# Performance work log

Hardware: AMD Instinct MI355X
Metric: run time of the kernel (lower is better)

Reference implementation:

```python
import jax, jax.numpy as jnp
import numpy as np

N = 50000   # num_nodes
E = 400000  # num_edges
IN, HID, OUT, H = 128, 64, 128, 4
GAT_HID = HID * H  # 256
EPS = 1e-5
NEG_SLOPE = 0.2


def setup_inputs() -> dict:
    key = jax.random.key(0)
    ks = jax.random.split(key, 24)

    def w(k, shape, fan_in):
        return (jax.random.normal(k, shape) * (1.0 / np.sqrt(fan_in))).astype(jnp.float32)

    x = jax.random.normal(ks[0], (N, IN), dtype=jnp.float32)
    edge_index = jax.random.randint(ks[1], (2, E), 0, N, dtype=jnp.int32)

    return {
        "x": x,
        "edge_index": edge_index,
        # GCN branch: layer1 IN->HID, layer2 HID->OUT
        "W_gcn1": w(ks[2], (IN, HID), IN), "b_gcn1": jnp.zeros((HID,), jnp.float32),
        "W_gcn2": w(ks[3], (HID, OUT), HID), "b_gcn2": jnp.zeros((OUT,), jnp.float32),
        # GAT branch: layer1 IN -> H heads x HID (concat), layer2 GAT_HID -> H heads x OUT (mean)
        "W_gat1": w(ks[4], (IN, H * HID), IN),
        "a_src1": w(ks[5], (H, HID), HID), "a_dst1": w(ks[6], (H, HID), HID),
        "b_gat1": jnp.zeros((H * HID,), jnp.float32),
        "W_gat2": w(ks[7], (GAT_HID, H * OUT), GAT_HID),
        "a_src2": w(ks[8], (H, OUT), OUT), "a_dst2": w(ks[9], (H, OUT), OUT),
        "b_gat2": jnp.zeros((OUT,), jnp.float32),
        # LayerNorms
        "g_gcn": jnp.ones((OUT,), jnp.float32), "bt_gcn": jnp.zeros((OUT,), jnp.float32),
        "g_gat": jnp.ones((OUT,), jnp.float32), "bt_gat": jnp.zeros((OUT,), jnp.float32),
        # projected_concat fusion
        "W_fuse": w(ks[10], (2 * OUT, OUT), 2 * OUT), "b_fuse": jnp.zeros((OUT,), jnp.float32),
    }


def _with_self_loops(src, dst, n):
    loop = jnp.arange(n, dtype=src.dtype)
    return jnp.concatenate([src, loop]), jnp.concatenate([dst, loop])


def _gcn_layer(x, W, b, src, dst, n):
    # PyG GCNConv: x' = D^{-1/2}(A+I)D^{-1/2} X W + b
    xw = x @ W
    s, d = _with_self_loops(src, dst, n)
    deg = jax.ops.segment_sum(jnp.ones_like(s, dtype=xw.dtype), d, num_segments=n)
    dis = jnp.where(deg > 0, jax.lax.rsqrt(jnp.maximum(deg, 1.0)), 0.0)
    norm = dis[s] * dis[d]                      # [E2]
    msg = norm[:, None] * xw[s]                 # [E2, C]
    return jax.ops.segment_sum(msg, d, num_segments=n) + b


def _segment_softmax(e, seg, n):
    m = jax.ops.segment_max(e, seg, num_segments=n)
    ee = jnp.exp(e - m[seg])
    den = jax.ops.segment_sum(ee, seg, num_segments=n)
    return ee / den[seg]


def _gat_layer(x, W, a_src, a_dst, b, src, dst, n, heads, out_ch, concat):
    xh = (x @ W).reshape(n, heads, out_ch)      # [N, H, C]
    alpha_s = jnp.einsum('nhc,hc->nh', xh, a_src)
    alpha_d = jnp.einsum('nhc,hc->nh', xh, a_dst)
    s, d = _with_self_loops(src, dst, n)
    e = jax.nn.leaky_relu(alpha_s[s] + alpha_d[d], NEG_SLOPE)   # [E2, H]
    alpha = _segment_softmax(e, d, n)                           # [E2, H]
    out = jax.ops.segment_sum(alpha[:, :, None] * xh[s], d, num_segments=n)  # [N,H,C]
    if concat:
        return out.reshape(n, heads * out_ch) + b
    return out.mean(axis=1) + b


def _layer_norm(x, g, b):
    mu = x.mean(axis=-1, keepdims=True)
    var = ((x - mu) ** 2).mean(axis=-1, keepdims=True)
    return (x - mu) * jax.lax.rsqrt(var + EPS) * g + b


def reference(x, edge_index,
              W_gcn1, b_gcn1, W_gcn2, b_gcn2,
              W_gat1, a_src1, a_dst1, b_gat1,
              W_gat2, a_src2, a_dst2, b_gat2,
              g_gcn, bt_gcn, g_gat, bt_gat,
              W_fuse, b_fuse):
    src, dst = edge_index[0], edge_index[1]
    n = x.shape[0]
    # GCN branch (relu between layers, dropout p=0.0 -> identity)
    h = jax.nn.relu(_gcn_layer(x, W_gcn1, b_gcn1, src, dst, n))
    x_gcn = _gcn_layer(h, W_gcn2, b_gcn2, src, dst, n)
    # GAT branch (elu between layers)
    g1 = _gat_layer(x, W_gat1, a_src1, a_dst1, b_gat1, src, dst, n, H, HID, True)
    g1 = jax.nn.elu(g1)
    x_gat = _gat_layer(g1, W_gat2, a_src2, a_dst2, b_gat2, src, dst, n, H, OUT, False)
    # Norm + projected_concat fusion
    x_gcn = _layer_norm(x_gcn, g_gcn, bt_gcn)
    x_gat = _layer_norm(x_gat, g_gat, bt_gat)
    x_cat = jnp.concatenate([x_gcn, x_gat], axis=-1)
    return x_cat @ W_fuse + b_fuse
```

## Files before the change

### kernel.cpp

```cpp
#include <hip/hip_runtime.h>
#include <cmath>

static constexpr float EPS = 1e-5f;
static constexpr float NEG = 0.2f;

typedef __attribute__((ext_vector_type(8))) short short8v;
typedef __attribute__((ext_vector_type(4))) short short4v;
typedef __attribute__((ext_vector_type(4))) float f32x4;
typedef __attribute__((ext_vector_type(2))) float f32x2;

__device__ inline unsigned short f2bf(float f) {
    union { float f; unsigned u; } v; v.f = f;
    unsigned r = v.u + 0x7FFF + ((v.u >> 16) & 1);
    return (unsigned short)(r >> 16);
}
__device__ inline float bf2f(unsigned short u) {
    union { unsigned u; float f; } v; v.u = (unsigned)u << 16; return v.f;
}

__global__ void setup_kernel(const int* __restrict__ ei, int* __restrict__ cnt, int E, int n,
                             const float* __restrict__ x, unsigned short* __restrict__ xb,
                             const float* W1, const float* W2, const float* W3,
                             const float* W4, const float* W5,
                             unsigned short* T1, unsigned short* T2, unsigned short* T3,
                             unsigned short* TF, unsigned short* T5,
                             const float* as1, const float* ad1,
                             const float* as2, const float* ad2,
                             float* wa1, float* wa2) {
    int gid = blockIdx.x * 256 + threadIdx.x;
    if (gid < E) {
        atomicAdd(&cnt[ei[E + gid]], 1);
        return;
    }
    gid -= E;
    int n32 = n * 32;
    if (gid < n32) {
        float4 v = *reinterpret_cast<const float4*>(&x[(size_t)gid * 4]);
        unsigned long long pk = (unsigned long long)f2bf(v.x)
                              | ((unsigned long long)f2bf(v.y) << 16)
                              | ((unsigned long long)f2bf(v.z) << 32)
                              | ((unsigned long long)f2bf(v.w) << 48);
        *reinterpret_cast<unsigned long long*>(&xb[(size_t)gid * 4]) = pk;
        return;
    }
    gid -= n32;
    if (gid < 212992) {
        int idx = gid;
        if (idx < 8192) {
            int c = idx / 128, k = idx % 128;
            T1[idx] = f2bf(W1[(size_t)k * 64 + c]);
        } else if (idx < 16384) {
            int j = idx - 8192, c = j / 64, k = j % 64;
            T2[j] = f2bf(W2[(size_t)k * 128 + c]);
        } else if (idx < 49152) {
            int j = idx - 16384, c = j / 128, k = j % 128;
            T3[j] = f2bf(W3[(size_t)k * 256 + c]);
        } else if (idx < 180224) {
            int j = idx - 49152;
            int c = j / 1024, kk = j % 1024, h = kk >> 8, k = kk & 255;
            TF[j] = f2bf(0.25f * W4[(size_t)k * 512 + h * 128 + c]);
        } else {
            int j = idx - 180224, c = j / 256, k = j % 256;
            T5[j] = f2bf(W5[(size_t)k * 128 + c]);
        }
        return;
    }
    gid -= 212992;
    if (gid < 1024) {
        int k = gid >> 3, t = gid & 7, h = t >> 1;
        const float* a = (t & 1) ? ad1 : as1;
        float s = 0.f;
        for (int c = 0; c < 64; c++) s += W3[(size_t)k * 256 + h * 64 + c] * a[h * 64 + c];
        wa1[gid] = s;
    } else if (gid < 3072) {
        int j = gid - 1024;
        int k = j >> 3, t = j & 7, h = t >> 1;
        const float* a = (t & 1) ? ad2 : as2;
        float s = 0.f;
        for (int c = 0; c < 128; c++) s += W4[(size_t)k * 512 + h * 128 + c] * a[h * 128 + c];
        wa2[j] = s;
    }
}

__global__ __launch_bounds__(256) void partial_kernel(const int* __restrict__ cnt,
                                                      int* __restrict__ partials, int n) {
    int tid = threadIdx.x, lane = tid & 63, wid = tid >> 6;
    int base = blockIdx.x * 1024 + tid * 4;
    int s = 0;
    if (base + 3 < n) {
        int4 v = *reinterpret_cast<const int4*>(&cnt[base]);
        s = v.x + v.y + v.z + v.w;
    } else {
        for (int j = 0; j < 4; j++) if (base + j < n) s += cnt[base + j];
    }
    #pragma unroll
    for (int o = 32; o; o >>= 1) s += __shfl_xor(s, o, 64);
    __shared__ int ws[4];
    if (lane == 0) ws[wid] = s;
    __syncthreads();
    if (tid == 0) partials[blockIdx.x] = ws[0] + ws[1] + ws[2] + ws[3];
}

__global__ void scanp_kernel(int* __restrict__ partials, int nb) {
    int lane = threadIdx.x;
    int v = (lane < nb) ? partials[lane] : 0;
    int s = v;
    #pragma unroll
    for (int o = 1; o < 64; o <<= 1) {
        int t = __shfl_up(s, o, 64);
        if (lane >= o) s += t;
    }
    if (lane < nb) partials[lane] = s - v;
}

__global__ __launch_bounds__(256) void scan2_kernel(const int* __restrict__ cnt,
                                                    const int* __restrict__ partials,
                                                    int* __restrict__ rowptr,
                                                    int* __restrict__ cursor,
                                                    float* __restrict__ dis, int n, int E) {
    int tid = threadIdx.x, lane = tid & 63, wid = tid >> 6;
    int base = blockIdx.x * 1024 + tid * 4;
    int v[4]; int s = 0;
    #pragma unroll
    for (int j = 0; j < 4; j++) { v[j] = (base + j < n) ? cnt[base + j] : 0; s += v[j]; }
    int ts = s;
    #pragma unroll
    for (int o = 1; o < 64; o <<= 1) {
        int t = __shfl_up(ts, o, 64);
        if (lane >= o) ts += t;
    }
    __shared__ int wsum[4];
    if (lane == 63) wsum[wid] = ts;
    __syncthreads();
    int woff = 0;
    for (int w = 0; w < wid; w++) woff += wsum[w];
    int excl = ts - s + woff + partials[blockIdx.x];
    #pragma unroll
    for (int j = 0; j < 4; j++) {
        int idx = base + j;
        if (idx < n) {
            rowptr[idx] = excl;
            cursor[idx] = excl;
            dis[idx] = rsqrtf((float)(v[j] + 1));
            excl += v[j];
        }
    }
    if (blockIdx.x == 0 && tid == 0) rowptr[n] = E;
}

__global__ void fill_kernel(const int* __restrict__ ei, int* __restrict__ cursor,
                            int* __restrict__ col, int E) {
    int e = blockIdx.x * 256 + threadIdx.x;
    if (e < E) {
        int d = ei[E + e];
        int pos = atomicAdd(&cursor[d], 1);
        col[pos] = ei[e];
    }
}

template<int BM, int K, int C, bool OBF, int ACT>
__global__ __launch_bounds__(256) void mfma_gemm(const unsigned short* __restrict__ A,
                                                 const unsigned short* __restrict__ WT,
                                                 const float* __restrict__ bias,
                                                 void* __restrict__ outp, int M) {
    constexpr int BN = 64, BK = 64;
    constexpr int MF = BM / 64;
    __shared__ unsigned short As[BM * BK];
    __shared__ unsigned short Ws[BN * BK];
    int tid = threadIdx.x;
    int wid = tid >> 6, lane = tid & 63;
    int m0 = blockIdx.x * BM;
    int n0 = blockIdx.y * BN;

    f32x4 acc[MF][4] = {};

    for (int k0 = 0; k0 < K; k0 += BK) {
        for (int i = tid; i < BM * (BK / 8); i += 256) {
            int row = i >> 3;
            int kk = (i & 7) * 8;
            int gr = m0 + row;
            short8v v = short8v{0, 0, 0, 0, 0, 0, 0, 0};
            if (gr < M) v = *reinterpret_cast<const short8v*>(&A[(size_t)gr * K + k0 + kk]);
            int byte = (kk * 2) ^ ((row & 7) << 4);
            *reinterpret_cast<short8v*>((char*)As + row * (BK * 2) + byte) = v;
        }
        for (int i = tid; i < BN * (BK / 8); i += 256) {
            int nrow = i >> 3;
            int kk = (i & 7) * 8;
            short8v v = *reinterpret_cast<const short8v*>(&WT[(size_t)(n0 + nrow) * K + k0 + kk]);
            int byte = (kk * 2) ^ ((nrow & 7) << 4);
            *reinterpret_cast<short8v*>((char*)Ws + nrow * (BK * 2) + byte) = v;
        }
        __syncthreads();
        #pragma unroll
        for (int kc = 0; kc < BK; kc += 32) {
            short8v afr[MF], bfr[4];
            int kk = kc + (lane >> 4) * 8;
            #pragma unroll
            for (int mf = 0; mf < MF; mf++) {
                int row = wid * (16 * MF) + mf * 16 + (lane & 15);
                int byte = (kk * 2) ^ ((row & 7) << 4);
                afr[mf] = *reinterpret_cast<const short8v*>((char*)As + row * (BK * 2) + byte);
            }
            #pragma unroll
            for (int nf = 0; nf < 4; nf++) {
                int nrow = nf * 16 + (lane & 15);
                int byte = (kk * 2) ^ ((nrow & 7) << 4);
                bfr[nf] = *reinterpret_cast<const short8v*>((char*)Ws + nrow * (BK * 2) + byte);
            }
            #pragma unroll
            for (int mf = 0; mf < MF; mf++)
                #pragma unroll
                for (int nf = 0; nf < 4; nf++)
                    acc[mf][nf] = __builtin_amdgcn_mfma_f32_16x16x32_bf16(
                        afr[mf], bfr[nf], acc[mf][nf], 0, 0, 0);
        }
        __syncthreads();
    }
    #pragma unroll
    for (int mf = 0; mf < MF; mf++) {
        #pragma unroll
        for (int nf = 0; nf < 4; nf++) {
            #pragma unroll
            for (int r = 0; r < 4; r++) {
                int row = m0 + wid * (16 * MF) + mf * 16 + (lane >> 4) * 4 + r;
                int colg = n0 + nf * 16 + (lane & 15);
                if (row < M) {
                    float v = acc[mf][nf][r];
                    if (bias) v += bias[colg];
                    if (ACT == 1) v = fmaxf(v, 0.f);
                    if constexpr (OBF)
                        ((unsigned short*)outp)[(size_t)row * C + colg] = f2bf(v);
                    else
                        ((float*)outp)[(size_t)row * C + colg] = v;
                }
            }
        }
    }
}

__global__ __launch_bounds__(256) void gemm_head_kernel(const unsigned short* __restrict__ A,
                                                        const unsigned short* __restrict__ WT3,
                                                        const float* __restrict__ bias,
                                                        unsigned short* __restrict__ g1b, int M) {
    constexpr int BM = 64, BK = 64, K = 128;
    int head = blockIdx.y;
    __shared__ unsigned short As[BM * BK];
    __shared__ unsigned short Ws[64 * BK];
    int tid = threadIdx.x;
    int wid = tid >> 6, lane = tid & 63;
    int m0 = blockIdx.x * BM;

    f32x4 acc[4] = {};

    for (int k0 = 0; k0 < K; k0 += BK) {
        for (int i = tid; i < BM * (BK / 8); i += 256) {
            int row = i >> 3;
            int kk = (i & 7) * 8;
            int gr = m0 + row;
            short8v v = short8v{0, 0, 0, 0, 0, 0, 0, 0};
            if (gr < M) v = *reinterpret_cast<const short8v*>(&A[(size_t)gr * 512 + head * 128 + k0 + kk]);
            int byte = (kk * 2) ^ ((row & 7) << 4);
            *reinterpret_cast<short8v*>((char*)As + row * (BK * 2) + byte) = v;
        }
        for (int i = tid; i < 64 * (BK / 8); i += 256) {
            int nrow = i >> 3;
            int kk = (i & 7) * 8;
            short8v v = *reinterpret_cast<const short8v*>(&WT3[(size_t)(head * 64 + nrow) * 128 + k0 + kk]);
            int byte = (kk * 2) ^ ((nrow & 7) << 4);
            *reinterpret_cast<short8v*>((char*)Ws + nrow * (BK * 2) + byte) = v;
        }
        __syncthreads();
        #pragma unroll
        for (int kc = 0; kc < BK; kc += 32) {
            short8v afr, bfr[4];
            int kk = kc + (lane >> 4) * 8;
            {
                int row = wid * 16 + (lane & 15);
                int byte = (kk * 2) ^ ((row & 7) << 4);
                afr = *reinterpret_cast<const short8v*>((char*)As + row * (BK * 2) + byte);
            }
            #pragma unroll
            for (int nf = 0; nf < 4; nf++) {
                int nrow = nf * 16 + (lane & 15);
                int byte = (kk * 2) ^ ((nrow & 7) << 4);
                bfr[nf] = *reinterpret_cast<const short8v*>((char*)Ws + nrow * (BK * 2) + byte);
            }
            #pragma unroll
            for (int nf = 0; nf < 4; nf++)
                acc[nf] = __builtin_amdgcn_mfma_f32_16x16x32_bf16(afr, bfr[nf], acc[nf], 0, 0, 0);
        }
        __syncthreads();
    }
    #pragma unroll
    for (int nf = 0; nf < 4; nf++) {
        #pragma unroll
        for (int r = 0; r < 4; r++) {
            int row = m0 + wid * 16 + (lane >> 4) * 4 + r;
            int cl = head * 64 + nf * 16 + (lane & 15);
            if (row < M) {
                float v = acc[nf][r] + bias[cl];
                v = v > 0.f ? v : __expf(v) - 1.f;
                g1b[(size_t)row * 256 + cl] = f2bf(v);
            }
        }
    }
}

template<int K>
__global__ __launch_bounds__(256) void gemm_ln_kernel(const unsigned short* __restrict__ A,
                                                      const unsigned short* __restrict__ WT,
                                                      const float* __restrict__ bias,
                                                      const float* __restrict__ gw,
                                                      const float* __restrict__ gb,
                                                      unsigned short* __restrict__ catb,
                                                      int coloff, int M) {
    constexpr int BM = 64, BN = 128, BK = 64;
    __shared__ unsigned short As[BM * BK];
    __shared__ unsigned short Ws[BN * BK];
    int tid = threadIdx.x;
    int wid = tid >> 6, lane = tid & 63;
    int m0 = blockIdx.x * BM;

    f32x4 acc[8] = {};

    for (int k0 = 0; k0 < K; k0 += BK) {
        for (int i = tid; i < BM * (BK / 8); i += 256) {
            int row = i >> 3;
            int kk = (i & 7) * 8;
            int gr = m0 + row;
            short8v v = short8v{0, 0, 0, 0, 0, 0, 0, 0};
            if (gr < M) v = *reinterpret_cast<const short8v*>(&A[(size_t)gr * K + k0 + kk]);
            int byte = (kk * 2) ^ ((row & 7) << 4);
            *reinterpret_cast<short8v*>((char*)As + row * (BK * 2) + byte) = v;
        }
        for (int i = tid; i < BN * (BK / 8); i += 256) {
            int nrow = i >> 3;
            int kk = (i & 7) * 8;
            short8v v = *reinterpret_cast<const short8v*>(&WT[(size_t)nrow * K + k0 + kk]);
            int byte = (kk * 2) ^ ((nrow & 7) << 4);
            *reinterpret_cast<short8v*>((char*)Ws + nrow * (BK * 2) + byte) = v;
        }
        __syncthreads();
        #pragma unroll
        for (int kc = 0; kc < BK; kc += 32) {
            short8v afr, bfr[8];
            int kk = kc + (lane >> 4) * 8;
            {
                int row = wid * 16 + (lane & 15);
                int byte = (kk * 2) ^ ((row & 7) << 4);
                afr = *reinterpret_cast<const short8v*>((char*)As + row * (BK * 2) + byte);
            }
            #pragma unroll
            for (int nf = 0; nf < 8; nf++) {
                int nrow = nf * 16 + (lane & 15);
                int byte = (kk * 2) ^ ((nrow & 7) << 4);
                bfr[nf] = *reinterpret_cast<const short8v*>((char*)Ws + nrow * (BK * 2) + byte);
            }
            #pragma unroll
            for (int nf = 0; nf < 8; nf++)
                acc[nf] = __builtin_amdgcn_mfma_f32_16x16x32_bf16(afr, bfr[nf], acc[nf], 0, 0, 0);
        }
        __syncthreads();
    }
    int cb = lane & 15;
    float gwv[8], gbv[8], bv[8];
    #pragma unroll
    for (int nf = 0; nf < 8; nf++) {
        int c = nf * 16 + cb;
        gwv[nf] = gw[c]; gbv[nf] = gb[c]; bv[nf] = bias[c];
    }
    #pragma unroll
    for (int r = 0; r < 4; r++) {
        int row = m0 + wid * 16 + (lane >> 4) * 4 + r;
        float v[8]; float sm = 0.f, sq = 0.f;
        #pragma unroll
        for (int nf = 0; nf < 8; nf++) {
            v[nf] = acc[nf][r] + bv[nf];
            sm += v[nf]; sq += v[nf] * v[nf];
        }
        #pragma unroll
        for (int o = 1; o < 16; o <<= 1) { sm += __shfl_xor(sm, o, 64); sq += __shfl_xor(sq, o, 64); }
        float mu = sm * (1.f / 128.f);
        float var = sq * (1.f / 128.f) - mu * mu;
        float rs = rsqrtf(var + EPS);
        if (row < M) {
            #pragma unroll
            for (int nf = 0; nf < 8; nf++)
                catb[(size_t)row * 256 + coloff + nf * 16 + cb] =
                    f2bf((v[nf] - mu) * rs * gwv[nf] + gbv[nf]);
        }
    }
}

template<int K>
__global__ __launch_bounds__(256) void alpha_x_kernel(const unsigned short* __restrict__ F,
                                                      const float* __restrict__ wa,
                                                      float* __restrict__ as_, float* __restrict__ ad_, int n) {
    constexpr int PL = K / 64;
    int wid = threadIdx.x >> 6, lane = threadIdx.x & 63;
    int node = blockIdx.x * 4 + wid;
    if (node >= n) return;
    float p[8] = {0, 0, 0, 0, 0, 0, 0, 0};
    const unsigned short* fr = F + (size_t)node * K + lane * PL;
    #pragma unroll
    for (int j = 0; j < PL; j++) {
        float v = bf2f(fr[j]);
        const float4* w4 = reinterpret_cast<const float4*>(wa + (size_t)(lane * PL + j) * 8);
        float4 wA = w4[0], wB = w4[1];
        p[0] += v * wA.x; p[1] += v * wA.y; p[2] += v * wA.z; p[3] += v * wA.w;
        p[4] += v * wB.x; p[5] += v * wB.y; p[6] += v * wB.z; p[7] += v * wB.w;
    }
    #pragma unroll
    for (int o = 1; o < 64; o <<= 1) {
        #pragma unroll
        for (int t = 0; t < 8; t++) p[t] += __shfl_xor(p[t], o, 64);
    }
    if (lane == 0) {
        #pragma unroll
        for (int t = 0; t < 8; t++) {
            if (t & 1) ad_[(size_t)node * 4 + (t >> 1)] = p[t];
            else       as_[(size_t)node * 4 + (t >> 1)] = p[t];
        }
    }
}

__global__ __launch_bounds__(256) void prop1_agg1_kernel(const unsigned short* __restrict__ xb,
                                                         const float* __restrict__ dis,
                                                         const float* __restrict__ as_,
                                                         const float* __restrict__ ad_,
                                                         const int* __restrict__ rowptr,
                                                         const int* __restrict__ col,
                                                         unsigned short* __restrict__ aggx,
                                                         unsigned short* __restrict__ agg,
                                                         int n) {
    constexpr int CAP = 96;
    __shared__ float ex[4][CAP][4];
    __shared__ float dsl[4][CAP];
    __shared__ int scol[4][CAP];
    int wid = threadIdx.x >> 6, lane = threadIdx.x & 63;
    int node = blockIdx.x * 4 + wid;
    if (node >= n) return;
    int b0 = rowptr[node];
    int cnt = rowptr[node + 1] - b0;
    float4 adv = *reinterpret_cast<const float4*>(&ad_[(size_t)node * 4]);
    float p0 = 0, p1 = 0, p2 = 0, p3 = 0;
    for (int i = lane; i <= cnt; i += 64) {
        int s = (i == cnt) ? node : col[b0 + i];
        float4 asv = *reinterpret_cast<const float4*>(&as_[(size_t)s * 4]);
        float e0 = asv.x + adv.x; e0 = e0 > 0.f ? e0 : NEG * e0; float x0 = __expf(e0);
        float e1 = asv.y + adv.y; e1 = e1 > 0.f ? e1 : NEG * e1; float x1 = __expf(e1);
        float e2 = asv.z + adv.z; e2 = e2 > 0.f ? e2 : NEG * e2; float x2 = __expf(e2);
        float e3 = asv.w + adv.w; e3 = e3 > 0.f ? e3 : NEG * e3; float x3 = __expf(e3);
        if (i < CAP) {
            ex[wid][i][0] = x0; ex[wid][i][1] = x1; ex[wid][i][2] = x2; ex[wid][i][3] = x3;
            scol[wid][i] = s;
            dsl[wid][i] = dis[s];
        }
        p0 += x0; p1 += x1; p2 += x2; p3 += x3;
    }
    #pragma unroll
    for (int o = 1; o < 64; o <<= 1) {
        p0 += __shfl_xor(p0, o, 64); p1 += __shfl_xor(p1, o, 64);
        p2 += __shfl_xor(p2, o, 64); p3 += __shfl_xor(p3, o, 64);
    }
    float inv0 = 1.f / p0, inv1 = 1.f / p1, inv2 = 1.f / p2, inv3 = 1.f / p3;
    for (int i = lane; i <= cnt && i < CAP; i += 64) {
        ex[wid][i][0] *= inv0; ex[wid][i][1] *= inv1;
        ex[wid][i][2] *= inv2; ex[wid][i][3] *= inv3;
    }
    __builtin_amdgcn_wave_barrier();
    f32x2 g2 = {0.f, 0.f};
    f32x2 ac2[4] = {};
    for (int i = 0; i <= cnt; i++) {
        int s; float w0, w1, w2, w3, dsv;
        if (i < CAP) {
            s = scol[wid][i];
            float4 e = *reinterpret_cast<const float4*>(&ex[wid][i][0]);
            w0 = e.x; w1 = e.y; w2 = e.z; w3 = e.w;
            dsv = dsl[wid][i];
        } else {
            s = (i == cnt) ? node : col[b0 + i];
            float4 asv = *reinterpret_cast<const float4*>(&as_[(size_t)s * 4]);
            float e0 = asv.x + adv.x; e0 = e0 > 0.f ? e0 : NEG * e0;
            float e1 = asv.y + adv.y; e1 = e1 > 0.f ? e1 : NEG * e1;
            float e2 = asv.z + adv.z; e2 = e2 > 0.f ? e2 : NEG * e2;
            float e3 = asv.w + adv.w; e3 = e3 > 0.f ? e3 : NEG * e3;
            w0 = __expf(e0) * inv0; w1 = __expf(e1) * inv1;
            w2 = __expf(e2) * inv2; w3 = __expf(e3) * inv3;
            dsv = dis[s];
        }
        unsigned gv = *reinterpret_cast<const unsigned*>(&xb[(size_t)s * 128 + lane * 2]);
        f32x2 f;
        f.x = bf2f((unsigned short)(gv & 0xFFFF));
        f.y = bf2f((unsigned short)(gv >> 16));
        g2 += dsv * f;
        ac2[0] += w0 * f;
        ac2[1] += w1 * f;
        ac2[2] += w2 * f;
        ac2[3] += w3 * f;
    }
    float dd = dis[node];
    unsigned pkg = (unsigned)f2bf(dd * g2.x) | ((unsigned)f2bf(dd * g2.y) << 16);
    *reinterpret_cast<unsigned*>(&aggx[(size_t)node * 128 + lane * 2]) = pkg;
    #pragma unroll
    for (int h = 0; h < 4; h++) {
        unsigned pk = (unsigned)f2bf(ac2[h].x) | ((unsigned)f2bf(ac2[h].y) << 16);
        *reinterpret_cast<unsigned*>(&agg[(size_t)node * 512 + h * 128 + lane * 2]) = pk;
    }
}

__global__ __launch_bounds__(256) void prop2_agg2_kernel(const unsigned short* __restrict__ g1b,
                                                         const unsigned short* __restrict__ hb,
                                                         const float* __restrict__ dis,
                                                         const float* __restrict__ as_,
                                                         const float* __restrict__ ad_,
                                                         const int* __restrict__ rowptr,
                                                         const int* __restrict__ col,
                                                         unsigned short* __restrict__ aggh,
                                                         unsigned short* __restrict__ agg,
                                                         int n) {
    constexpr int CAP = 96;
    __shared__ float ex[4][CAP][4];
    __shared__ float dsl[4][CAP];
    __shared__ int scol[4][CAP];
    int wid = threadIdx.x >> 6, lane = threadIdx.x & 63;
    int node = blockIdx.x * 4 + wid;
    if (node >= n) return;
    int b0 = rowptr[node];
    int cnt = rowptr[node + 1] - b0;
    float4 adv = *reinterpret_cast<const float4*>(&ad_[(size_t)node * 4]);
    float p0 = 0, p1 = 0, p2 = 0, p3 = 0;
    for (int i = lane; i <= cnt; i += 64) {
        int s = (i == cnt) ? node : col[b0 + i];
        float4 asv = *reinterpret_cast<const float4*>(&as_[(size_t)s * 4]);
        float e0 = asv.x + adv.x; e0 = e0 > 0.f ? e0 : NEG * e0; float x0 = __expf(e0);
        float e1 = asv.y + adv.y; e1 = e1 > 0.f ? e1 : NEG * e1; float x1 = __expf(e1);
        float e2 = asv.z + adv.z; e2 = e2 > 0.f ? e2 : NEG * e2; float x2 = __expf(e2);
        float e3 = asv.w + adv.w; e3 = e3 > 0.f ? e3 : NEG * e3; float x3 = __expf(e3);
        if (i < CAP) {
            ex[wid][i][0] = x0; ex[wid][i][1] = x1; ex[wid][i][2] = x2; ex[wid][i][3] = x3;
            scol[wid][i] = s;
            dsl[wid][i] = dis[s];
        }
        p0 += x0; p1 += x1; p2 += x2; p3 += x3;
    }
    #pragma unroll
    for (int o = 1; o < 64; o <<= 1) {
        p0 += __shfl_xor(p0, o, 64); p1 += __shfl_xor(p1, o, 64);
        p2 += __shfl_xor(p2, o, 64); p3 += __shfl_xor(p3, o, 64);
    }
    float inv0 = 1.f / p0, inv1 = 1.f / p1, inv2 = 1.f / p2, inv3 = 1.f / p3;
    for (int i = lane; i <= cnt && i < CAP; i += 64) {
        ex[wid][i][0] *= inv0; ex[wid][i][1] *= inv1;
        ex[wid][i][2] *= inv2; ex[wid][i][3] *= inv3;
    }
    __builtin_amdgcn_wave_barrier();
    float hacc = 0.f;
    f32x2 ac2[4][2] = {};
    for (int i = 0; i <= cnt; i++) {
        int s; float w0, w1, w2, w3, dsv;
        if (i < CAP) {
            s = scol[wid][i];
            float4 e = *reinterpret_cast<const float4*>(&ex[wid][i][0]);
            w0 = e.x; w1 = e.y; w2 = e.z; w3 = e.w;
            dsv = dsl[wid][i];
        } else {
            s = (i == cnt) ? node : col[b0 + i];
            float4 asv = *reinterpret_cast<const float4*>(&as_[(size_t)s * 4]);
            float e0 = asv.x + adv.x; e0 = e0 > 0.f ? e0 : NEG * e0;
            float e1 = asv.y + adv.y; e1 = e1 > 0.f ? e1 : NEG * e1;
            float e2 = asv.z + adv.z; e2 = e2 > 0.f ? e2 : NEG * e2;
            float e3 = asv.w + adv.w; e3 = e3 > 0.f ? e3 : NEG * e3;
            w0 = __expf(e0) * inv0; w1 = __expf(e1) * inv1;
            w2 = __expf(e2) * inv2; w3 = __expf(e3) * inv3;
            dsv = dis[s];
        }
        short4v v = *reinterpret_cast<const short4v*>(&g1b[(size_t)s * 256 + lane * 4]);
        float hv = bf2f(hb[(size_t)s * 64 + lane]);
        hacc += dsv * hv;
        f32x2 fa, fb;
        fa.x = bf2f((unsigned short)v[0]); fa.y = bf2f((unsigned short)v[1]);
        fb.x = bf2f((unsigned short)v[2]); fb.y = bf2f((unsigned short)v[3]);
        ac2[0][0] += w0 * fa; ac2[0][1] += w0 * fb;
        ac2[1][0] += w1 * fa; ac2[1][1] += w1 * fb;
        ac2[2][0] += w2 * fa; ac2[2][1] += w2 * fb;
        ac2[3][0] += w3 * fa; ac2[3][1] += w3 * fb;
    }
    float dd = dis[node];
    aggh[(size_t)node * 64 + lane] = f2bf(dd * hacc);
    #pragma unroll
    for (int h = 0; h < 4; h++) {
        short4v o4;
        o4[0] = (short)f2bf(ac2[h][0].x); o4[1] = (short)f2bf(ac2[h][0].y);
        o4[2] = (short)f2bf(ac2[h][1].x); o4[3] = (short)f2bf(ac2[h][1].y);
        *reinterpret_cast<short4v*>(&agg[(size_t)node * 1024 + h * 256 + lane * 4]) = o4;
    }
}

extern "C" void kernel_launch(void* const* d_in, const int* in_sizes, int n_in,
                              void* d_out, int out_size, void* d_ws, size_t ws_size,
                              hipStream_t stream) {
    const float* x      = (const float*)d_in[0];
    const int*   ei     = (const int*)d_in[1];
    const float* W_gcn1 = (const float*)d_in[2];
    const float* b_gcn1 = (const float*)d_in[3];
    const float* W_gcn2 = (const float*)d_in[4];
    const float* b_gcn2 = (const float*)d_in[5];
    const float* W_gat1 = (const float*)d_in[6];
    const float* a_src1 = (const float*)d_in[7];
    const float* a_dst1 = (const float*)d_in[8];
    const float* b_gat1 = (const float*)d_in[9];
    const float* W_gat2 = (const float*)d_in[10];
    const float* a_src2 = (const float*)d_in[11];
    const float* a_dst2 = (const float*)d_in[12];
    const float* b_gat2 = (const float*)d_in[13];
    const float* g_gcn  = (const float*)d_in[14];
    const float* bt_gcn = (const float*)d_in[15];
    const float* g_gat  = (const float*)d_in[16];
    const float* bt_gat = (const float*)d_in[17];
    const float* W_fuse = (const float*)d_in[18];
    const float* b_fuse = (const float*)d_in[19];
    float* out = (float*)d_out;

    const int n = in_sizes[0] / 128;
    const int E = in_sizes[1] / 2;

    char* ws = (char*)d_ws;
    size_t off = 0;
    auto alloc = [&](size_t bytes) -> char* {
        char* p = ws + off;
        off += (bytes + 255) & ~(size_t)255;
        return p;
    };
    int*   cnt      = (int*)alloc((size_t)n * 4);
    int*   rowptr   = (int*)alloc((size_t)(n + 1) * 4);
    int*   cursor   = (int*)alloc((size_t)n * 4);
    int*   col      = (int*)alloc((size_t)E * 4);
    int*   partials = (int*)alloc(64 * 4);
    float* dis      = (float*)alloc((size_t)n * 4);
    float* as_      = (float*)alloc((size_t)n * 16);
    float* ad_      = (float*)alloc((size_t)n * 16);
    float* wa1      = (float*)alloc(1024 * 4);
    float* wa2      = (float*)alloc(2048 * 4);
    unsigned short* xb   = (unsigned short*)alloc((size_t)n * 128 * 2);
    unsigned short* WT1  = (unsigned short*)alloc(8192 * 2);
    unsigned short* WT2  = (unsigned short*)alloc(8192 * 2);
    unsigned short* WT3  = (unsigned short*)alloc(32768 * 2);
    unsigned short* WTF  = (unsigned short*)alloc(131072 * 2);
    unsigned short* WT5  = (unsigned short*)alloc(32768 * 2);
    unsigned short* BIG   = (unsigned short*)alloc((size_t)n * 1024 * 2);
    unsigned short* agg2b = BIG;
    unsigned short* agg1b = BIG;
    unsigned short* aggx1 = BIG + (size_t)n * 512;
    unsigned short* hb    = (unsigned short*)alloc((size_t)n * 64 * 2);
    unsigned short* aggh  = (unsigned short*)alloc((size_t)n * 64 * 2);
    unsigned short* g1b   = (unsigned short*)alloc((size_t)n * 256 * 2);
    unsigned short* catb  = (unsigned short*)alloc((size_t)n * 256 * 2);

    const int nb = (n + 1023) / 1024;

    hipMemsetAsync(cnt, 0, (size_t)n * 4, stream);
    {
        long long total = (long long)E + (long long)n * 32 + 212992 + 3072;
        int blocks = (int)((total + 255) / 256);
        setup_kernel<<<blocks, 256, 0, stream>>>(ei, cnt, E, n, x, xb,
            W_gcn1, W_gcn2, W_gat1, W_gat2, W_fuse, WT1, WT2, WT3, WTF, WT5,
            a_src1, a_dst1, a_src2, a_dst2, wa1, wa2);
    }
    partial_kernel<<<nb, 256, 0, stream>>>(cnt, partials, n);
    scanp_kernel<<<1, 64, 0, stream>>>(partials, nb);
    scan2_kernel<<<nb, 256, 0, stream>>>(cnt, partials, rowptr, cursor, dis, n, E);
    fill_kernel<<<(E + 255) / 256, 256, 0, stream>>>(ei, cursor, col, E);

    int gm64 = (n + 63) / 64;
    int gn4 = (n + 3) / 4;

    alpha_x_kernel<128><<<gn4, 256, 0, stream>>>(xb, wa1, as_, ad_, n);
    prop1_agg1_kernel<<<gn4, 256, 0, stream>>>(xb, dis, as_, ad_, rowptr, col, aggx1, agg1b, n);
    mfma_gemm<64, 128, 64, true, 1><<<dim3(gm64, 1), 256, 0, stream>>>(aggx1, WT1, b_gcn1, hb, n);
    gemm_head_kernel<<<dim3(gm64, 4), 256, 0, stream>>>(agg1b, WT3, b_gat1, g1b, n);
    alpha_x_kernel<256><<<gn4, 256, 0, stream>>>(g1b, wa2, as_, ad_, n);
    prop2_agg2_kernel<<<gn4, 256, 0, stream>>>(g1b, hb, dis, as_, ad_, rowptr, col, aggh, agg2b, n);
    gemm_ln_kernel<64><<<gm64, 256, 0, stream>>>(aggh, WT2, b_gcn2, g_gcn, bt_gcn, catb, 0, n);
    gemm_ln_kernel<1024><<<gm64, 256, 0, stream>>>(agg2b, WTF, b_gat2, g_gat, bt_gat, catb, 128, n);

    mfma_gemm<64, 256, 128, false, 0><<<dim3(gm64, 2), 256, 0, stream>>>(catb, WT5, b_fuse, out, n);
}
```

Measured before the change: 351.2 us.

## Unroll gather loops by two and prescale GCN hidden by source degree norm

The two propagation kernels now process two neighbours per iteration, issuing both gathers before accumulating so more memory loads are in flight. In prop2 the per-edge dis[s] multiply is removed by folding the source normalisation into the first GEMM epilogue through a new rowscale argument. The shared-memory cache of dis values is dropped and the LDS cache capacity shrinks from 96 to 64 entries, which may raise occupancy. The cost is that nodes above 64 neighbours take the recompute path more often, and prop1 now reads dis[s] from global memory on every edge.

```diff
diff --git a/kernel.cpp b/kernel.cpp
--- a/kernel.cpp
+++ b/kernel.cpp
@@ -162,6 +162,7 @@
 __global__ __launch_bounds__(256) void mfma_gemm(const unsigned short* __restrict__ A,
                                                  const unsigned short* __restrict__ WT,
                                                  const float* __restrict__ bias,
+                                                 const float* __restrict__ rowscale,
                                                  void* __restrict__ outp, int M) {
     constexpr int BN = 64, BK = 64;
     constexpr int MF = BM / 64;
@@ -229,6 +230,7 @@
                     float v = acc[mf][nf][r];
                     if (bias) v += bias[colg];
                     if (ACT == 1) v = fmaxf(v, 0.f);
+                    if (rowscale) v *= rowscale[row];
                     if constexpr (OBF)
                         ((unsigned short*)outp)[(size_t)row * C + colg] = f2bf(v);
                     else
@@ -434,9 +436,8 @@
                                                          unsigned short* __restrict__ aggx,
                                                          unsigned short* __restrict__ agg,
                                                          int n) {
-    constexpr int CAP = 96;
+    constexpr int CAP = 64;
     __shared__ float ex[4][CAP][4];
-    __shared__ float dsl[4][CAP];
     __shared__ int scol[4][CAP];
     int wid = threadIdx.x >> 6, lane = threadIdx.x & 63;
     int node = blockIdx.x * 4 + wid;
@@ -455,7 +456,6 @@
         if (i < CAP) {
             ex[wid][i][0] = x0; ex[wid][i][1] = x1; ex[wid][i][2] = x2; ex[wid][i][3] = x3;
             scol[wid][i] = s;
-            dsl[wid][i] = dis[s];
         }
         p0 += x0; p1 += x1; p2 += x2; p3 += x3;
     }
@@ -470,15 +470,11 @@
         ex[wid][i][2] *= inv2; ex[wid][i][3] *= inv3;
     }
     __builtin_amdgcn_wave_barrier();
-    f32x2 g2 = {0.f, 0.f};
-    f32x2 ac2[4] = {};
-    for (int i = 0; i <= cnt; i++) {
-        int s; float w0, w1, w2, w3, dsv;
+
+    auto fetchw = [&](int i, int &s, float4 &w) {
         if (i < CAP) {
             s = scol[wid][i];
-            float4 e = *reinterpret_cast<const float4*>(&ex[wid][i][0]);
-            w0 = e.x; w1 = e.y; w2 = e.z; w3 = e.w;
-            dsv = dsl[wid][i];
+            w = *reinterpret_cast<const float4*>(&ex[wid][i][0]);
         } else {
             s = (i == cnt) ? node : col[b0 + i];
             float4 asv = *reinterpret_cast<const float4*>(&as_[(size_t)s * 4]);
@@ -486,19 +482,41 @@
             float e1 = asv.y + adv.y; e1 = e1 > 0.f ? e1 : NEG * e1;
             float e2 = asv.z + adv.z; e2 = e2 > 0.f ? e2 : NEG * e2;
             float e3 = asv.w + adv.w; e3 = e3 > 0.f ? e3 : NEG * e3;
-            w0 = __expf(e0) * inv0; w1 = __expf(e1) * inv1;
-            w2 = __expf(e2) * inv2; w3 = __expf(e3) * inv3;
-            dsv = dis[s];
-        }
-        unsigned gv = *reinterpret_cast<const unsigned*>(&xb[(size_t)s * 128 + lane * 2]);
-        f32x2 f;
-        f.x = bf2f((unsigned short)(gv & 0xFFFF));
-        f.y = bf2f((unsigned short)(gv >> 16));
-        g2 += dsv * f;
-        ac2[0] += w0 * f;
-        ac2[1] += w1 * f;
-        ac2[2] += w2 * f;
-        ac2[3] += w3 * f;
+            w = make_float4(__expf(e0) * inv0, __expf(e1) * inv1,
+                            __expf(e2) * inv2, __expf(e3) * inv3);
+        }
+    };
+
+    f32x2 g2 = {0.f, 0.f};
+    f32x2 ac2[4] = {};
+    int total = cnt + 1;
+    int i = 0;
+    for (; i + 1 < total; i += 2) {
+        int s0, s1; float4 wa, wb;
+        fetchw(i, s0, wa);
+        fetchw(i + 1, s1, wb);
+        float ds0 = dis[s0], ds1 = dis[s1];
+        unsigned gv0 = *reinterpret_cast<const unsigned*>(&xb[(size_t)s0 * 128 + lane * 2]);
+        unsigned gv1 = *reinterpret_cast<const unsigned*>(&xb[(size_t)s1 * 128 + lane * 2]);
+        f32x2 f0, f1;
+        f0.x = bf2f((unsigned short)(gv0 & 0xFFFF)); f0.y = bf2f((unsigned short)(gv0 >> 16));
+        f1.x = bf2f((unsigned short)(gv1 & 0xFFFF)); f1.y = bf2f((unsigned short)(gv1 >> 16));
+        g2 += ds0 * f0;      g2 += ds1 * f1;
+        ac2[0] += wa.x * f0; ac2[0] += wb.x * f1;
+        ac2[1] += wa.y * f0; ac2[1] += wb.y * f1;
+        ac2[2] += wa.z * f0; ac2[2] += wb.z * f1;
+        ac2[3] += wa.w * f0; ac2[3] += wb.w * f1;
+    }
+    if (i < total) {
+        int s0; float4 wa;
+        fetchw(i, s0, wa);
+        float ds0 = dis[s0];
+        unsigned gv0 = *reinterpret_cast<const unsigned*>(&xb[(size_t)s0 * 128 + lane * 2]);
+        f32x2 f0;
+        f0.x = bf2f((unsigned short)(gv0 & 0xFFFF)); f0.y = bf2f((unsigned short)(gv0 >> 16));
+        g2 += ds0 * f0;
+        ac2[0] += wa.x * f0; ac2[1] += wa.y * f0;
+        ac2[2] += wa.z * f0; ac2[3] += wa.w * f0;
     }
     float dd = dis[node];
     unsigned pkg = (unsigned)f2bf(dd * g2.x) | ((unsigned)f2bf(dd * g2.y) << 16);
@@ -511,7 +529,7 @@
 }
 
 __global__ __launch_bounds__(256) void prop2_agg2_kernel(const unsigned short* __restrict__ g1b,
-                                                         const unsigned short* __restrict__ hb,
+                                                         const unsigned short* __restrict__ hbs,
                                                          const float* __restrict__ dis,
                                                          const float* __restrict__ as_,
                                                          const float* __restrict__ ad_,
@@ -520,9 +538,8 @@
                                                          unsigned short* __restrict__ aggh,
                                                          unsigned short* __restrict__ agg,
                                                          int n) {
-    constexpr int CAP = 96;
+    constexpr int CAP = 64;
     __shared__ float ex[4][CAP][4];
-    __shared__ float dsl[4][CAP];
     __shared__ int scol[4][CAP];
     int wid = threadIdx.x >> 6, lane = threadIdx.x & 63;
     int node = blockIdx.x * 4 + wid;
@@ -541,7 +558,6 @@
         if (i < CAP) {
             ex[wid][i][0] = x0; ex[wid][i][1] = x1; ex[wid][i][2] = x2; ex[wid][i][3] = x3;
             scol[wid][i] = s;
-            dsl[wid][i] = dis[s];
         }
         p0 += x0; p1 += x1; p2 += x2; p3 += x3;
     }
@@ -556,15 +572,11 @@
         ex[wid][i][2] *= inv2; ex[wid][i][3] *= inv3;
     }
     __builtin_amdgcn_wave_barrier();
-    float hacc = 0.f;
-    f32x2 ac2[4][2] = {};
-    for (int i = 0; i <= cnt; i++) {
-        int s; float w0, w1, w2, w3, dsv;
+
+    auto fetchw = [&](int i, int &s, float4 &w) {
         if (i < CAP) {
             s = scol[wid][i];
-            float4 e = *reinterpret_cast<const float4*>(&ex[wid][i][0]);
-            w0 = e.x; w1 = e.y; w2 = e.z; w3 = e.w;
-            dsv = dsl[wid][i];
+            w = *reinterpret_cast<const float4*>(&ex[wid][i][0]);
         } else {
             s = (i == cnt) ? node : col[b0 + i];
             float4 asv = *reinterpret_cast<const float4*>(&as_[(size_t)s * 4]);
@@ -572,20 +584,50 @@
             float e1 = asv.y + adv.y; e1 = e1 > 0.f ? e1 : NEG * e1;
             float e2 = asv.z + adv.z; e2 = e2 > 0.f ? e2 : NEG * e2;
             float e3 = asv.w + adv.w; e3 = e3 > 0.f ? e3 : NEG * e3;
-            w0 = __expf(e0) * inv0; w1 = __expf(e1) * inv1;
-            w2 = __expf(e2) * inv2; w3 = __expf(e3) * inv3;
-            dsv = dis[s];
-        }
-        short4v v = *reinterpret_cast<const short4v*>(&g1b[(size_t)s * 256 + lane * 4]);
-        float hv = bf2f(hb[(size_t)s * 64 + lane]);
-        hacc += dsv * hv;
-        f32x2 fa, fb;
-        fa.x = bf2f((unsigned short)v[0]); fa.y = bf2f((unsigned short)v[1]);
-        fb.x = bf2f((unsigned short)v[2]); fb.y = bf2f((unsigned short)v[3]);
-        ac2[0][0] += w0 * fa; ac2[0][1] += w0 * fb;
-        ac2[1][0] += w1 * fa; ac2[1][1] += w1 * fb;
-        ac2[2][0] += w2 * fa; ac2[2][1] += w2 * fb;
-        ac2[3][0] += w3 * fa; ac2[3][1] += w3 * fb;
+            w = make_float4(__expf(e0) * inv0, __expf(e1) * inv1,
+                            __expf(e2) * inv2, __expf(e3) * inv3);
+        }
+    };
+
+    float hacc = 0.f;
+    f32x2 ac2[4][2] = {};
+    int total = cnt + 1;
+    int i = 0;
+    for (; i + 1 < total; i += 2) {
+        int s0, s1; float4 wa, wb;
+        fetchw(i, s0, wa);
+        fetchw(i + 1, s1, wb);
+        short4v v0 = *reinterpret_cast<const short4v*>(&g1b[(size_t)s0 * 256 + lane * 4]);
+        short4v v1 = *reinterpret_cast<const short4v*>(&g1b[(size_t)s1 * 256 + lane * 4]);
+        float hv0 = bf2f(hbs[(size_t)s0 * 64 + lane]);
+        float hv1 = bf2f(hbs[(size_t)s1 * 64 + lane]);
+        hacc += hv0 + hv1;
+        f32x2 fa0, fb0, fa1, fb1;
+        fa0.x = bf2f((unsigned short)v0[0]); fa0.y = bf2f((unsigned short)v0[1]);
+        fb0.x = bf2f((unsigned short)v0[2]); fb0.y = bf2f((unsigned short)v0[3]);
+        fa1.x = bf2f((unsigned short)v1[0]); fa1.y = bf2f((unsigned short)v1[1]);
+        fb1.x = bf2f((unsigned short)v1[2]); fb1.y = bf2f((unsigned short)v1[3]);
+        ac2[0][0] += wa.x * fa0; ac2[0][1] += wa.x * fb0;
+        ac2[0][0] += wb.x * fa1; ac2[0][1] += wb.x * fb1;
+        ac2[1][0] += wa.y * fa0; ac2[1][1] += wa.y * fb0;
+        ac2[1][0] += wb.y * fa1; ac2[1][1] += wb.y * fb1;
+        ac2[2][0] += wa.z * fa0; ac2[2][1] += wa.z * fb0;
+        ac2[2][0] += wb.z * fa1; ac2[2][1] += wb.z * fb1;
+        ac2[3][0] += wa.w * fa0; ac2[3][1] += wa.w * fb0;
+        ac2[3][0] += wb.w * fa1; ac2[3][1] += wb.w * fb1;
+    }
+    if (i < total) {
+        int s0; float4 wa;
+        fetchw(i, s0, wa);
+        short4v v0 = *reinterpret_cast<const short4v*>(&g1b[(size_t)s0 * 256 + lane * 4]);
+        hacc += bf2f(hbs[(size_t)s0 * 64 + lane]);
+        f32x2 fa0, fb0;
+        fa0.x = bf2f((unsigned short)v0[0]); fa0.y = bf2f((unsigned short)v0[1]);
+        fb0.x = bf2f((unsigned short)v0[2]); fb0.y = bf2f((unsigned short)v0[3]);
+        ac2[0][0] += wa.x * fa0; ac2[0][1] += wa.x * fb0;
+        ac2[1][0] += wa.y * fa0; ac2[1][1] += wa.y * fb0;
+        ac2[2][0] += wa.z * fa0; ac2[2][1] += wa.z * fb0;
+        ac2[3][0] += wa.w * fa0; ac2[3][1] += wa.w * fb0;
     }
     float dd = dis[node];
     aggh[(size_t)node * 64 + lane] = f2bf(dd * hacc);
@@ -653,7 +695,7 @@
     unsigned short* agg2b = BIG;
     unsigned short* agg1b = BIG;
     unsigned short* aggx1 = BIG + (size_t)n * 512;
-    unsigned short* hb    = (unsigned short*)alloc((size_t)n * 64 * 2);
+    unsigned short* hbs   = (unsigned short*)alloc((size_t)n * 64 * 2);
     unsigned short* aggh  = (unsigned short*)alloc((size_t)n * 64 * 2);
     unsigned short* g1b   = (unsigned short*)alloc((size_t)n * 256 * 2);
     unsigned short* catb  = (unsigned short*)alloc((size_t)n * 256 * 2);
@@ -678,12 +720,12 @@
 
     alpha_x_kernel<128><<<gn4, 256, 0, stream>>>(xb, wa1, as_, ad_, n);
     prop1_agg1_kernel<<<gn4, 256, 0, stream>>>(xb, dis, as_, ad_, rowptr, col, aggx1, agg1b, n);
-    mfma_gemm<64, 128, 64, true, 1><<<dim3(gm64, 1), 256, 0, stream>>>(aggx1, WT1, b_gcn1, hb, n);
+    mfma_gemm<64, 128, 64, true, 1><<<dim3(gm64, 1), 256, 0, stream>>>(aggx1, WT1, b_gcn1, dis, hbs, n);
     gemm_head_kernel<<<dim3(gm64, 4), 256, 0, stream>>>(agg1b, WT3, b_gat1, g1b, n);
     alpha_x_kernel<256><<<gn4, 256, 0, stream>>>(g1b, wa2, as_, ad_, n);
-    prop2_agg2_kernel<<<gn4, 256, 0, stream>>>(g1b, hb, dis, as_, ad_, rowptr, col, aggh, agg2b, n);
+    prop2_agg2_kernel<<<gn4, 256, 0, stream>>>(g1b, hbs, dis, as_, ad_, rowptr, col, aggh, agg2b, n);
     gemm_ln_kernel<64><<<gm64, 256, 0, stream>>>(aggh, WT2, b_gcn2, g_gcn, bt_gcn, catb, 0, n);
     gemm_ln_kernel<1024><<<gm64, 256, 0, stream>>>(agg2b, WTF, b_gat2, g_gat, bt_gat, catb, 128, n);
 
-    mfma_gemm<64, 256, 128, false, 0><<<dim3(gm64, 2), 256, 0, stream>>>(catb, WT5, b_fuse, out, n);
-}
+    mfma_gemm<64, 256, 128, false, 0><<<dim3(gm64, 2), 256, 0, stream>>>(catb, WT5, b_fuse, nullptr, out, n);
+}
```

Result: faster. 343.9 us (-2.1%).
